# Performance work log

Measured on AMD Instinct MI355X. Metric: run time of the kernel, lower is better.

## Reference

```python
import jax, jax.numpy as jnp
import numpy as np

B = 128
IN = 256
NLVL = 6
KLVL = 3
CH = 4
C = 4 * CH * CH          # 64 channels per node
OU = 8                   # out_filter_siz_u
OV = 8                   # out_filter_siz_v
NK = 2 ** KLVL           # 8 leaf nodes per axis
W_SCALE = 1.0 / 16.0     # ~1/sqrt(2*2*C) so 7 stacked relu-convs stay numerically sane


def setup_inputs() -> dict:
    key = jax.random.key(0)
    ks = jax.random.split(key, 2 * NLVL + 4)
    fx = IN // 2 ** NLVL  # 4: input patch filter size
    inp = {}
    inp["in_data"] = jax.random.normal(ks[0], (B, IN, IN, 1), jnp.float32)
    inp["in_filter"] = jax.random.normal(ks[1], (fx, fx, 1, C), jnp.float32) * W_SCALE
    inp["in_bias"] = jnp.zeros((C,), jnp.float32)
    i = 2
    for lvl in range(1, NLVL + 1):
        n = 2 ** min(lvl, KLVL)  # node grid: grows to 2^klvl then stays
        inp[f"f{lvl}"] = jax.random.normal(ks[i], (n, n, 2, 2, C, C), jnp.float32) * W_SCALE
        inp[f"b{lvl}"] = jnp.zeros((n, n, C), jnp.float32)
        i += 1
    inp["Wd"] = jax.random.normal(ks[i], (NK, NK, 2, C, OU * OV), jnp.float32) * W_SCALE
    return inp


def _node_conv(x, w, b):
    # x: [Nu,Nv,B,H,W,C]; w: [Nu,Nv,2,2,C,C]; 2x2 stride-2 VALID conv per node
    Nu, Nv, Bn, H, W, Cc = x.shape
    xr = x.reshape(Nu, Nv, Bn, H // 2, 2, W // 2, 2, Cc)
    y = jnp.einsum('uvbhxwyc,uvxyco->uvbhwo', xr, w)
    return jax.nn.relu(y + b[:, :, None, None, None, :])


def _forward(in_data, in_filter, in_bias, fs, bs, Wd):
    Bn = in_data.shape[0]
    fx, fy = in_filter.shape[0], in_filter.shape[1]
    # input interp conv: stride == kernel -> non-overlapping patch GEMM
    xr = in_data[..., 0].reshape(Bn, in_data.shape[1] // fx, fx, in_data.shape[2] // fy, fy)
    x = jax.nn.relu(jnp.einsum('bxpyq,pqc->bxyc', xr, in_filter[:, :, 0, :]) + in_bias)
    x = x[None, None]  # [1,1,B,2^nlvl,2^nlvl,C] node grid
    for lvl in range(1, NLVL + 1):
        if lvl <= KLVL:
            # children (itu,itv) read parent (itu//2, itv//2)
            x = jnp.repeat(jnp.repeat(x, 2, axis=0), 2, axis=1)
        x = _node_conv(x, fs[lvl - 1], bs[lvl - 1])
    feats = x[:, :, :, 0, 0, :]  # [NK,NK,B,C]; spatial is 1x1 at level nlvl
    out = jnp.einsum('uvbc,uvrck->uvbrk', feats, Wd)  # r in {real, imag}
    out = out.reshape(NK, NK, Bn, 2, OU, OV)
    out = jnp.transpose(out, (2, 0, 4, 1, 5, 3))  # [B,itu,ou,itv,ov,2]
    return out.reshape(Bn, NK * OU, NK * OV, 2)


def reference(in_data, in_filter, in_bias, f1, b1, f2, b2, f3, b3, f4, b4, f5, b5, f6, b6, Wd):
    fs = (f1, f2, f3, f4, f5, f6)
    bs = (b1, b2, b3, b4, b5, b6)
    return _forward(in_data, in_filter, in_bias, fs, bs, Wd)
```

## Files before the change

### kernel.cpp

```cpp
#include <hip/hip_runtime.h>
#include <hip/hip_bf16.h>
#include <cstdint>
#include <cstddef>


typedef __attribute__((ext_vector_type(8))) short short8;
typedef __attribute__((ext_vector_type(4))) float f32x4;
typedef unsigned short ushort_t;

static __device__ __forceinline__ float b2f(const __hip_bfloat16 x) {
    return __bfloat162float(x);
}
static __device__ __forceinline__ ushort_t f2bf(float x) {
    __hip_bfloat16 h = __float2bfloat16(x);
    ushort_t u;
    __builtin_memcpy(&u, &h, 2);
    return u;
}
static __device__ __forceinline__ void gl_lds16(const void* g, void* l) {
    __builtin_amdgcn_global_load_lds(
        (const __attribute__((address_space(1))) void*)g,
        (__attribute__((address_space(3))) void*)l, 16, 0, 0);
}
#define WAIT_LGKM0() __builtin_amdgcn_s_waitcnt(0xC07F)
#define WAIT_VM0()   __builtin_amdgcn_s_waitcnt(0x0F70)

#define PREP_BLOCKS 2533

static __device__ __forceinline__ void prep_work(
    int gid, int isbf,
    const void* f1, const void* f2, const void* f3,
    const void* f4, const void* f5, const void* f6, const void* wdsrc,
    const void* b1, const void* b2, const void* b3,
    const void* b4, const void* b5, const void* b6,
    ushort_t* __restrict__ wbuf, ushort_t* __restrict__ wdbuf,
    float* __restrict__ bbuf)
{
    if (gid >= 648448) return;
    if (gid >= 630784) {
        const int bg = gid - 630784;
        const void* src; int base;
        if      (bg <   256) { src = b1; base = 0;     }
        else if (bg <  1280) { src = b2; base = 256;   }
        else if (bg <  5376) { src = b3; base = 1280;  }
        else if (bg <  9472) { src = b4; base = 5376;  }
        else if (bg < 13568) { src = b5; base = 9472;  }
        else                 { src = b6; base = 13568; }
        const int local = bg - base;
        bbuf[bg] = isbf ? b2f(((const __hip_bfloat16*)src)[local])
                        : ((const float*)src)[local];
        return;
    }
    if (gid >= 565248) {
        const int local = gid - 565248;
        const int lane = local & 63;
        const int slot = (local >> 6) & 15;
        const int site = local >> 10;
        const int ks2 = slot >> 3, nh = slot & 7, q = lane >> 4;
        const int n = nh * 16 + (lane & 15);
        const int r = n >> 6, kk = n & 63;
        const int cbase = ks2 * 32 + q * 8;
        ushort_t pk[8];
        if (isbf) {
            const ushort_t* s = (const ushort_t*)wdsrc;
            #pragma unroll
            for (int j = 0; j < 8; j++)
                pk[j] = s[(((size_t)(site * 2 + r) * 64 + cbase + j) * 64) + kk];
        } else {
            const float* s = (const float*)wdsrc;
            #pragma unroll
            for (int j = 0; j < 8; j++)
                pk[j] = f2bf(s[(((size_t)(site * 2 + r) * 64 + cbase + j) * 64) + kk]);
        }
        *(uint4*)&wdbuf[(size_t)local * 8] = *(uint4*)pk;
        return;
    }
    const void* fsrc; int base;
    if      (gid <   8192) { fsrc = f1; base = 0;      }
    else if (gid <  40960) { fsrc = f2; base = 8192;   }
    else if (gid < 172032) { fsrc = f3; base = 40960;  }
    else if (gid < 303104) { fsrc = f4; base = 172032; }
    else if (gid < 434176) { fsrc = f5; base = 303104; }
    else                   { fsrc = f6; base = 434176; }
    const int local = gid - base;
    const int lane = local & 63;
    const int slot = (local >> 6) & 7;
    const int sitetap = local >> 9;
    const int ks = slot >> 2, nh = slot & 3, q = lane >> 4;
    const int n = (lane & 15) + nh * 16;
    const int kbase = ks * 32 + q * 8;
    ushort_t pk[8];
    if (isbf) {
        const ushort_t* s = (const ushort_t*)fsrc + (size_t)sitetap * 4096;
        #pragma unroll
        for (int j = 0; j < 8; j++) pk[j] = s[(kbase + j) * 64 + n];
    } else {
        const float* s = (const float*)fsrc + (size_t)sitetap * 4096;
        #pragma unroll
        for (int j = 0; j < 8; j++) pk[j] = f2bf(s[(kbase + j) * 64 + n]);
    }
    *(uint4*)&wbuf[(size_t)gid * 8] = *(uint4*)pk;
}

static __device__ __forceinline__ void stage0_body(
    int blk, int isbf,
    const void* __restrict__ in_data, const void* __restrict__ filt,
    const void* __restrict__ bias, __hip_bfloat16* __restrict__ x0,
    int b_off, int Bc)
{
    const int X  = blk & 63;
    const int bl = blk >> 6;
    const int bg = bl + b_off;

    __shared__ float sIn[4][256];
    __shared__ float sF[16][64];
    __shared__ float sB[64];

    const int t = threadIdx.x;
    const size_t srow = ((size_t)bg * 256 + (size_t)X * 4) * 256;

    if (isbf) {
        const __hip_bfloat16* src = (const __hip_bfloat16*)in_data + srow;
        #pragma unroll
        for (int i = 0; i < 4; i++) {
            int flat = i * 256 + t;
            int p = flat >> 8, col = flat & 255;
            sIn[p][col] = b2f(src[(size_t)p * 256 + col]);
        }
        const __hip_bfloat16* fsrc = (const __hip_bfloat16*)filt;
        #pragma unroll
        for (int i = 0; i < 4; i++) {
            int flat = i * 256 + t;
            sF[flat >> 6][flat & 63] = b2f(fsrc[flat]);
        }
        if (t < 64) sB[t] = b2f(((const __hip_bfloat16*)bias)[t]);
    } else {
        const float* src = (const float*)in_data + srow;
        const int p = t >> 6, c4 = (t & 63) * 4;
        *(float4*)&sIn[p][c4] = *(const float4*)(src + (size_t)p * 256 + c4);
        const float* fsrc = (const float*)filt;
        #pragma unroll
        for (int i = 0; i < 4; i++) {
            int flat = i * 256 + t;
            sF[flat >> 6][flat & 63] = fsrc[flat];
        }
        if (t < 64) sB[t] = ((const float*)bias)[t];
    }
    __syncthreads();

    const int ty = t >> 4;
    const int tc = t & 15;

    float acc[4][4];
    {
        const float4 bv = *(const float4*)&sB[tc * 4];
        #pragma unroll
        for (int yi = 0; yi < 4; yi++) {
            acc[yi][0] = bv.x; acc[yi][1] = bv.y;
            acc[yi][2] = bv.z; acc[yi][3] = bv.w;
        }
    }

    #pragma unroll
    for (int p = 0; p < 4; p++) {
        float4 rin[4], rf[4];
        #pragma unroll
        for (int yi = 0; yi < 4; yi++)
            rin[yi] = *(const float4*)&sIn[p][ty * 16 + yi * 4];
        #pragma unroll
        for (int q = 0; q < 4; q++)
            rf[q] = *(const float4*)&sF[p * 4 + q][tc * 4];
        #pragma unroll
        for (int yi = 0; yi < 4; yi++) {
            #pragma unroll
            for (int q = 0; q < 4; q++) {
                const float a = ((const float*)&rin[yi])[q];
                acc[yi][0] = fmaf(a, rf[q].x, acc[yi][0]);
                acc[yi][1] = fmaf(a, rf[q].y, acc[yi][1]);
                acc[yi][2] = fmaf(a, rf[q].z, acc[yi][2]);
                acc[yi][3] = fmaf(a, rf[q].w, acc[yi][3]);
            }
        }
    }

    ushort_t* dst = (ushort_t*)x0;
    #pragma unroll
    for (int yi = 0; yi < 4; yi++) {
        uint2 pk;
        pk.x = (uint32_t)f2bf(fmaxf(acc[yi][0], 0.f))
             | ((uint32_t)f2bf(fmaxf(acc[yi][1], 0.f)) << 16);
        pk.y = (uint32_t)f2bf(fmaxf(acc[yi][2], 0.f))
             | ((uint32_t)f2bf(fmaxf(acc[yi][3], 0.f)) << 16);
        const int wpos = ty * 4 + yi;
        *(uint2*)(dst + ((size_t)(X * 64 + wpos) * Bc + bl) * 64 + tc * 4) = pk;
    }
}

__global__ __launch_bounds__(256) void k_prep0(
    const void* __restrict__ in_data,
    const void* f1, const void* f2, const void* f3,
    const void* f4, const void* f5, const void* f6, const void* wdsrc,
    const void* b1, const void* b2, const void* b3,
    const void* b4, const void* b5, const void* b6,
    ushort_t* __restrict__ wbuf, ushort_t* __restrict__ wdbuf,
    float* __restrict__ bbuf, int* __restrict__ flag,
    const void* __restrict__ filt, const void* __restrict__ bias0,
    __hip_bfloat16* __restrict__ x0, int Bc)
{
    __shared__ int sflag;
    const int t = threadIdx.x;
    if (t < 64) {
        const float v = __uint_as_float(((const uint32_t*)in_data)[t]);
        const bool plaus = (v == 0.0f) || (fabsf(v) > 1e-8f && fabsf(v) < 1e4f);
        const unsigned long long m = __ballot(plaus);
        if (t == 0) sflag = (__popcll(m) >= 48) ? 0 : 1;
    }
    __syncthreads();
    const int isbf = sflag;

    if (blockIdx.x < PREP_BLOCKS) {
        if (blockIdx.x == 0 && t == 0) *flag = isbf;
        prep_work(blockIdx.x * 256 + t, isbf,
                  f1, f2, f3, f4, f5, f6, wdsrc,
                  b1, b2, b3, b4, b5, b6, wbuf, wdbuf, bbuf);
    } else {
        stage0_body(blockIdx.x - PREP_BLOCKS, isbf, in_data, filt, bias0, x0, 0, Bc);
    }
}

__global__ __launch_bounds__(256) void k_stage0(
    const void* __restrict__ in_data, const void* __restrict__ filt,
    const void* __restrict__ bias, __hip_bfloat16* __restrict__ x0,
    const int* __restrict__ flag, int b_off, int Bc)
{
    stage0_body(blockIdx.x, *flag, in_data, filt, bias, x0, b_off, Bc);
}

__global__ __launch_bounds__(256, 2) void k_level4(
    const __hip_bfloat16* __restrict__ xin,
    const ushort_t* __restrict__ wbuf,
    const float* __restrict__ bbuf,
    __hip_bfloat16* __restrict__ xout,
    int Nv_out, int HW, int Bc, int mtiles)
{
    __shared__ ushort_t smem[17408];

    int idx = blockIdx.x;
    const int mt = idx % mtiles; idx /= mtiles;
    const int w  = idx % HW; idx /= HW;
    const int h  = idx % HW; idx /= HW;
    const int Nv_in = Nv_out >> 1;
    const int vp = idx % Nv_in;
    const int up = idx / Nv_in;

    const int t = threadIdx.x;
    const int wave = t >> 6, lane = t & 63;
    const int lm = lane & 15, lq = lane >> 4;

    const int so = (2 * up + (wave >> 1)) * Nv_out + (2 * vp + (wave & 1));
    const int H_in = HW * 2;
    const size_t pstride = (size_t)Bc * 64;
    const size_t siteb = (size_t)(up * Nv_in + vp) * H_in * H_in * pstride;
    const ushort_t* wsite = wbuf + (size_t)so * 4 * 4096 + lane * 8;

    {
        const int hi = 2 * h + (wave >> 1), wi = 2 * w + (wave & 1);
        const size_t tapoff = siteb + ((size_t)hi * H_in + wi) * pstride;
        #pragma unroll
        for (int j = 0; j < 8; j++) {
            const int ks = j >> 2, mh = j & 3;
            int b = mt * 64 + mh * 16 + lm;
            if (b >= Bc) b = Bc - 1;
            gl_lds16(xin + tapoff + (size_t)b * 64 + ks * 32 + lq * 8,
                     &smem[(wave * 8 + j) * 512]);
        }
    }

    short8 breg[32];
    #pragma unroll
    for (int s = 0; s < 32; s++)
        breg[s] = *(const short8*)(wsite + s * 512);

    float bv[4];
    #pragma unroll
    for (int fn = 0; fn < 4; fn++) bv[fn] = bbuf[so * 64 + fn * 16 + lm];

    __syncthreads();

    const f32x4 zero = {0.f, 0.f, 0.f, 0.f};
    f32x4 acc[4][4];
    #pragma unroll
    for (int i = 0; i < 4; i++)
        #pragma unroll
        for (int j = 0; j < 4; j++) acc[i][j] = zero;

    #pragma unroll
    for (int tap = 0; tap < 4; tap++) {
        #pragma unroll
        for (int ks = 0; ks < 2; ks++) {
            #pragma unroll
            for (int fm = 0; fm < 4; fm++) {
                short8 a = *(const short8*)&smem[(tap * 8 + ks * 4 + fm) * 512 + lane * 8];
                #pragma unroll
                for (int fn = 0; fn < 4; fn++)
                    acc[fm][fn] = __builtin_amdgcn_mfma_f32_16x16x32_bf16(
                        a, breg[tap * 8 + ks * 4 + fn], acc[fm][fn], 0, 0, 0);
            }
        }
    }
    __syncthreads();

    ushort_t* so_buf = smem + wave * 4352;
    #pragma unroll
    for (int fm = 0; fm < 4; fm++) {
        #pragma unroll
        for (int fn = 0; fn < 4; fn++) {
            #pragma unroll
            for (int r = 0; r < 4; r++) {
                const int row = fm * 16 + lq * 4 + r;
                so_buf[row * 68 + fn * 16 + lm] =
                    f2bf(fmaxf(acc[fm][fn][r] + bv[fn], 0.f));
            }
        }
    }
    __syncthreads();

    const size_t obase = ((size_t)so * HW * HW + (size_t)h * HW + w) * pstride;
    #pragma unroll
    for (int i = 0; i < 8; i++) {
        const int task = i * 64 + lane;
        const int oct = task & 7, row = task >> 3;
        const int b = mt * 64 + row;
        if (b < Bc) {
            *(uint4*)(xout + obase + (size_t)b * 64 + oct * 8) =
                *(const uint4*)&so_buf[row * 68 + oct * 8];
        }
    }
}

__global__ __launch_bounds__(256) void k_f456(
    const __hip_bfloat16* __restrict__ xin,
    const ushort_t* __restrict__ w4, const ushort_t* __restrict__ w5,
    const ushort_t* __restrict__ w6, const ushort_t* __restrict__ wd,
    const float* __restrict__ b4, const float* __restrict__ b5,
    const float* __restrict__ b6,
    void* __restrict__ out, const int* __restrict__ flag,
    int Bc, int b_off, int mtiles)
{
    const int isbf = *flag;
    const int bx = blockIdx.x;
    const int mt = bx % mtiles;
    const int site = bx / mtiles;
    const int u = site >> 3, v = site & 7;

    __shared__ ushort_t smem[37376];

    const int t = threadIdx.x;
    const int wv = t >> 6, lane = t & 63;
    const int lm = lane & 15, lq = lane >> 4;

    const ushort_t* w6s = w6 + (size_t)site * 16384 + lane * 8;
    const ushort_t* wds = wd + (size_t)site * 8192  + lane * 8;

    float bv4[4], bv5[4];
    #pragma unroll
    for (int fn = 0; fn < 4; fn++) {
        bv4[fn] = b4[site * 64 + fn * 16 + lm];
        bv5[fn] = b5[site * 64 + fn * 16 + lm];
    }
    const float bv6 = b6[site * 64 + wv * 16 + lm];

    {
        const ushort_t* w4s = w4 + (size_t)site * 16384;
        #pragma unroll
        for (int s2 = 0; s2 < 8; s2++) {
            const int s = wv * 8 + s2;
            gl_lds16(w4s + s * 512 + lane * 8, &smem[s * 512]);
        }
    }
    __syncthreads();

    const f32x4 zero = {0.f, 0.f, 0.f, 0.f};
    const int h5 = wv >> 1, w5p = wv & 1;
    ushort_t* mid1w = smem + 16384 + wv * 4224;
    ushort_t* Aw = smem + 33280 + wv * 1024;
    const size_t pstride = (size_t)Bc * 64;

    int brow = mt * 16 + lm;
    if (brow >= Bc) brow = Bc - 1;
    const __hip_bfloat16* xbase =
        xin + (size_t)site * 64 * pstride + (size_t)brow * 64 + lq * 8;

    for (int i = 0; i < 4; i++) {
        const int h4 = 2 * h5 + (i >> 1), w4p = 2 * w5p + (i & 1);
        f32x4 acc[4];
        #pragma unroll
        for (int b_ = 0; b_ < 4; b_++) acc[b_] = zero;

        for (int tap = 0; tap < 4; tap++) {
            const int h3 = 2 * h4 + (tap >> 1), w3 = 2 * w4p + (tap & 1);
            const size_t poff = (size_t)(h3 * 8 + w3) * pstride;
            WAIT_LGKM0();
            #pragma unroll
            for (int ks = 0; ks < 2; ks++) {
                gl_lds16(xbase + poff + ks * 32, &Aw[ks * 512]);
            }
            WAIT_VM0();
            __builtin_amdgcn_sched_barrier(0);
            #pragma unroll
            for (int ks = 0; ks < 2; ks++) {
                short8 a = *(const short8*)&Aw[ks * 512 + lane * 8];
                #pragma unroll
                for (int fn = 0; fn < 4; fn++) {
                    short8 bfr = *(const short8*)&smem[(tap * 8 + ks * 4 + fn) * 512 + lane * 8];
                    acc[fn] = __builtin_amdgcn_mfma_f32_16x16x32_bf16(a, bfr, acc[fn], 0, 0, 0);
                }
            }
        }
        #pragma unroll
        for (int fn = 0; fn < 4; fn++) {
            #pragma unroll
            for (int r = 0; r < 4; r++) {
                const int m = lq * 4 + r;
                const int ch = fn * 16 + lm;
                mid1w[m * 264 + i * 64 + ch] =
                    f2bf(fmaxf(acc[fn][r] + bv4[fn], 0.f));
            }
        }
    }
    __syncthreads();

    {
        const ushort_t* w5s = w5 + (size_t)site * 16384;
        #pragma unroll
        for (int s2 = 0; s2 < 8; s2++) {
            const int s = wv * 8 + s2;
            gl_lds16(w5s + s * 512 + lane * 8, &smem[s * 512]);
        }
    }
    __syncthreads();

    short8 b3r[8];
    short8 wdr[4];
    {
        f32x4 acc2[4];
        #pragma unroll
        for (int b_ = 0; b_ < 4; b_++) acc2[b_] = zero;

        #pragma unroll
        for (int i = 0; i < 4; i++) {
            #pragma unroll
            for (int ks = 0; ks < 2; ks++) {
                short8 a0 = *(const short8*)&mid1w[lm * 264 + i * 64 + ks * 32 + lq * 8];
                #pragma unroll
                for (int fn = 0; fn < 4; fn++) {
                    short8 bfr = *(const short8*)&smem[(i * 8 + ks * 4 + fn) * 512 + lane * 8];
                    acc2[fn] = __builtin_amdgcn_mfma_f32_16x16x32_bf16(a0, bfr, acc2[fn], 0, 0, 0);
                }
            }
        }

        #pragma unroll
        for (int tap = 0; tap < 4; tap++)
            #pragma unroll
            for (int ks = 0; ks < 2; ks++)
                b3r[tap * 2 + ks] = *(const short8*)(w6s + (tap * 8 + ks * 4 + wv) * 512);
        #pragma unroll
        for (int ks = 0; ks < 2; ks++)
            #pragma unroll
            for (int n2 = 0; n2 < 2; n2++)
                wdr[ks * 2 + n2] = *(const short8*)(wds + (ks * 8 + 2 * wv + n2) * 512);

        #pragma unroll
        for (int fn = 0; fn < 4; fn++) {
            #pragma unroll
            for (int r = 0; r < 4; r++) {
                const int m = lq * 4 + r;
                const int ch = fn * 16 + lm;
                mid1w[m * 72 + ch] =
                    f2bf(fmaxf(acc2[fn][r] + bv5[fn], 0.f));
            }
        }
    }
    __syncthreads();

    {
        f32x4 acc3 = zero;
        #pragma unroll
        for (int tap = 0; tap < 4; tap++) {
            const ushort_t* sl = smem + 16384 + tap * 4224;
            #pragma unroll
            for (int ks = 0; ks < 2; ks++) {
                short8 a0 = *(const short8*)&sl[lm * 72 + ks * 32 + lq * 8];
                acc3 = __builtin_amdgcn_mfma_f32_16x16x32_bf16(a0, b3r[tap * 2 + ks], acc3, 0, 0, 0);
            }
        }
        ushort_t* mid3 = smem + 33280;
        #pragma unroll
        for (int r = 0; r < 4; r++) {
            const int m = lq * 4 + r;
            const int ch = wv * 16 + lm;
            mid3[m * 72 + ch] = f2bf(fmaxf(acc3[r] + bv6, 0.f));
        }
    }
    __syncthreads();

    {
        const ushort_t* mid3 = smem + 33280;
        f32x4 acc4[2];
        acc4[0] = zero; acc4[1] = zero;
        #pragma unroll
        for (int ks = 0; ks < 2; ks++) {
            short8 a0 = *(const short8*)&mid3[lm * 72 + ks * 32 + lq * 8];
            #pragma unroll
            for (int n2 = 0; n2 < 2; n2++) {
                acc4[n2] = __builtin_amdgcn_mfma_f32_16x16x32_bf16(a0, wdr[ks * 2 + n2], acc4[n2], 0, 0, 0);
            }
        }
        #pragma unroll
        for (int n2 = 0; n2 < 2; n2++) {
            const int n = (2 * wv + n2) * 16 + lm;
            const int rr = n >> 6, ou = (n >> 3) & 7, ov = n & 7;
            const size_t obase =
                (((size_t)(u * 8 + ou)) * 64 + (v * 8 + ov)) * 2 + rr;
            #pragma unroll
            for (int reg = 0; reg < 4; reg++) {
                const int brw = mt * 16 + lq * 4 + reg;
                if (brw < Bc) {
                    const size_t oidx = obase + (size_t)(b_off + brw) * 8192;
                    if (isbf) ((__hip_bfloat16*)out)[oidx] =
                        __float2bfloat16(acc4[n2][reg]);
                    else ((float*)out)[oidx] = acc4[n2][reg];
                }
            }
        }
    }
}

extern "C" void kernel_launch(void* const* d_in, const int* in_sizes, int n_in,
                              void* d_out, int out_size, void* d_ws, size_t ws_size,
                              hipStream_t stream)
{
    (void)in_sizes; (void)n_in; (void)out_size;

    const void* in_data = d_in[0];
    const void* filt    = d_in[1];
    const void* bias0   = d_in[2];
    const void* fl[7];
    const void* bl[7];
    for (int l = 1; l <= 6; l++) {
        fl[l] = d_in[1 + 2 * l];
        bl[l] = d_in[2 + 2 * l];
    }
    const void* Wd = d_in[15];

    const int Bfull = 128;
    const size_t perB = (size_t)64 * 64 * 64;

    const size_t wbufBytes  = 565248ull * 16;
    const size_t wdbufBytes = 65536ull * 16;
    const size_t bbufBytes  = 17664ull * 4;
    const size_t headBytes  = 256 + wbufBytes + wdbufBytes + bbufBytes;

    const size_t avail = ws_size > headBytes ? ws_size - headBytes : 0;
    int Bc = 0;
    for (int c = 128; c >= 1; c >>= 1) {
        if ((size_t)2 * c * perB * sizeof(__hip_bfloat16) <= avail) { Bc = c; break; }
    }
    if (Bc == 0) return;

    int* flag = (int*)d_ws;
    ushort_t* wbuf  = (ushort_t*)((char*)d_ws + 256);
    ushort_t* wdbuf = (ushort_t*)((char*)d_ws + 256 + wbufBytes);
    float* bbuf = (float*)((char*)d_ws + 256 + wbufBytes + wdbufBytes);
    __hip_bfloat16* bufA = (__hip_bfloat16*)((char*)d_ws + headBytes);
    __hip_bfloat16* bufB = bufA + (size_t)Bc * perB;

    static const size_t w_off[7] = {0, 0, 65536, 327680, 1376256, 2424832, 3473408};
    static const int    b_off_tab[7] = {0, 0, 256, 1280, 5376, 9472, 13568};

    const int mt4 = (Bc + 63) / 64;
    const int mt16 = (Bc + 15) / 16;

    for (int b_off = 0; b_off < Bfull; b_off += Bc) {
        if (b_off == 0) {
            k_prep0<<<dim3(PREP_BLOCKS + Bc * 64), 256, 0, stream>>>(
                in_data,
                fl[1], fl[2], fl[3], fl[4], fl[5], fl[6], Wd,
                bl[1], bl[2], bl[3], bl[4], bl[5], bl[6],
                wbuf, wdbuf, bbuf, flag,
                filt, bias0, bufA, Bc);
        } else {
            k_stage0<<<dim3(Bc * 64), 256, 0, stream>>>(in_data, filt, bias0, bufA, flag, b_off, Bc);
        }

        __hip_bfloat16* cur = bufA;
        __hip_bfloat16* nxt = bufB;
        for (int lvl = 1; lvl <= 3; lvl++) {
            const int Nu = 1 << lvl;
            const int H  = 64 >> lvl;
            const int Nv_in = Nu >> 1;
            dim3 grid(Nv_in * Nv_in * H * H * mt4);
            k_level4<<<grid, 256, 0, stream>>>(cur, wbuf + w_off[lvl],
                bbuf + b_off_tab[lvl], nxt, Nu, H, Bc, mt4);
            __hip_bfloat16* tmp = cur; cur = nxt; nxt = tmp;
        }

        k_f456<<<dim3(64 * mt16), 256, 0, stream>>>(cur,
            wbuf + w_off[4], wbuf + w_off[5], wbuf + w_off[6], wdbuf,
            bbuf + b_off_tab[4], bbuf + b_off_tab[5], bbuf + b_off_tab[6],
            d_out, flag, Bc, b_off, mt16);
    }
}
```

Baseline: 249.2 us.

## Fuse tree levels 1 and 2 into one kernel via LDS intermediate

Adds a k_fused12 kernel that computes level-1 and level-2 node convolutions in one pass. Each block loads a 4x4 spatial patch of stage-0 output, keeps the level-1 results in LDS, and then computes the 16 level-2 sites directly. This removes one kernel launch and the global write and re-read of the level-1 activations. In exchange the block uses more LDS, holds 32 weight fragments in registers per wave, and uses smaller 16-row batch tiles, which could lower occupancy.

```diff
diff --git a/kernel.cpp b/kernel.cpp
--- a/kernel.cpp
+++ b/kernel.cpp
@@ -236,6 +236,143 @@
     stage0_body(blockIdx.x, *flag, in_data, filt, bias, x0, b_off, Bc);
 }
 
+__global__ __launch_bounds__(256, 2) void k_fused12(
+    const __hip_bfloat16* __restrict__ xin,
+    const ushort_t* __restrict__ w1,
+    const ushort_t* __restrict__ w2,
+    const float* __restrict__ b1, const float* __restrict__ b2,
+    __hip_bfloat16* __restrict__ xout,
+    int Bc, int mtiles)
+{
+    __shared__ __align__(16) ushort_t smem[34816];
+
+    int idx = blockIdx.x;
+    const int mt = idx % mtiles; idx /= mtiles;
+    const int w2p = idx & 15;
+    const int h2p = idx >> 4;
+
+    const int t = threadIdx.x;
+    const int wave = t >> 6, lane = t & 63;
+    const int lm = lane & 15, lq = lane >> 4;
+
+    const size_t pstride = (size_t)Bc * 64;
+
+    {
+        int brow = mt * 16 + lm;
+        if (brow >= Bc) brow = Bc - 1;
+        #pragma unroll
+        for (int k = 0; k < 4; k++) {
+            const int p = wave * 4 + k;
+            const int i = p >> 2, j = p & 3;
+            const size_t poff =
+                ((size_t)(4 * h2p + i) * 64 + (4 * w2p + j)) * pstride;
+            #pragma unroll
+            for (int ks = 0; ks < 2; ks++) {
+                gl_lds16(xin + poff + (size_t)brow * 64 + ks * 32 + lq * 8,
+                         &smem[(p * 2 + ks) * 512]);
+            }
+        }
+    }
+
+    const ushort_t* w1site = w1 + (size_t)wave * 16384 + lane * 8;
+    short8 breg[32];
+    #pragma unroll
+    for (int s = 0; s < 32; s++) breg[s] = *(const short8*)(w1site + s * 512);
+
+    float bv1[4];
+    #pragma unroll
+    for (int fn = 0; fn < 4; fn++) bv1[fn] = b1[wave * 64 + fn * 16 + lm];
+
+    __syncthreads();
+
+    const f32x4 zero = {0.f, 0.f, 0.f, 0.f};
+    ushort_t* l1b = smem + 16384;
+
+    #pragma unroll
+    for (int ab = 0; ab < 4; ab++) {
+        const int a = ab >> 1, b = ab & 1;
+        f32x4 acc[4];
+        #pragma unroll
+        for (int fn = 0; fn < 4; fn++) acc[fn] = zero;
+
+        #pragma unroll
+        for (int cd = 0; cd < 4; cd++) {
+            const int p = (2 * a + (cd >> 1)) * 4 + (2 * b + (cd & 1));
+            #pragma unroll
+            for (int ks = 0; ks < 2; ks++) {
+                short8 afr = *(const short8*)&smem[(p * 2 + ks) * 512 + lane * 8];
+                #pragma unroll
+                for (int fn = 0; fn < 4; fn++)
+                    acc[fn] = __builtin_amdgcn_mfma_f32_16x16x32_bf16(
+                        afr, breg[cd * 8 + ks * 4 + fn], acc[fn], 0, 0, 0);
+            }
+        }
+        ushort_t* dst = l1b + (wave * 4 + ab) * 1152;
+        #pragma unroll
+        for (int fn = 0; fn < 4; fn++) {
+            #pragma unroll
+            for (int r = 0; r < 4; r++) {
+                const int m = lq * 4 + r;
+                dst[m * 72 + fn * 16 + lm] =
+                    f2bf(fmaxf(acc[fn][r] + bv1[fn], 0.f));
+            }
+        }
+    }
+    __syncthreads();
+
+    ushort_t* so_buf = smem + wave * 2176;
+    for (int k = 0; k < 4; k++) {
+        const int s2 = wave * 4 + k;
+        const int u2 = s2 >> 2, v2 = s2 & 3;
+        const int s1p = (u2 >> 1) * 2 + (v2 >> 1);
+        const ushort_t* w2site = w2 + (size_t)s2 * 16384 + lane * 8;
+
+        f32x4 acc[4];
+        #pragma unroll
+        for (int fn = 0; fn < 4; fn++) acc[fn] = zero;
+
+        #pragma unroll
+        for (int ab = 0; ab < 4; ab++) {
+            const ushort_t* sl = l1b + (s1p * 4 + ab) * 1152;
+            #pragma unroll
+            for (int ks = 0; ks < 2; ks++) {
+                short8 afr = *(const short8*)&sl[lm * 72 + ks * 32 + lq * 8];
+                #pragma unroll
+                for (int fn = 0; fn < 4; fn++) {
+                    short8 bfr = *(const short8*)(w2site + (ab * 8 + ks * 4 + fn) * 512);
+                    acc[fn] = __builtin_amdgcn_mfma_f32_16x16x32_bf16(
+                        afr, bfr, acc[fn], 0, 0, 0);
+                }
+            }
+        }
+
+        float bv2[4];
+        #pragma unroll
+        for (int fn = 0; fn < 4; fn++) bv2[fn] = b2[s2 * 64 + fn * 16 + lm];
+
+        #pragma unroll
+        for (int fn = 0; fn < 4; fn++) {
+            #pragma unroll
+            for (int r = 0; r < 4; r++) {
+                const int m = lq * 4 + r;
+                so_buf[m * 68 + fn * 16 + lm] =
+                    f2bf(fmaxf(acc[fn][r] + bv2[fn], 0.f));
+            }
+        }
+        const size_t obase = ((size_t)s2 * 256 + h2p * 16 + w2p) * pstride;
+        #pragma unroll
+        for (int i2 = 0; i2 < 2; i2++) {
+            const int task = i2 * 64 + lane;
+            const int oct = task & 7, row = task >> 3;
+            const int brw = mt * 16 + row;
+            if (brw < Bc) {
+                *(uint4*)(xout + obase + (size_t)brw * 64 + oct * 8) =
+                    *(const uint4*)&so_buf[row * 68 + oct * 8];
+            }
+        }
+    }
+}
+
 __global__ __launch_bounds__(256, 2) void k_level4(
     const __hip_bfloat16* __restrict__ xin,
     const ushort_t* __restrict__ wbuf,
@@ -243,7 +380,7 @@
     __hip_bfloat16* __restrict__ xout,
     int Nv_out, int HW, int Bc, int mtiles)
 {
-    __shared__ ushort_t smem[17408];
+    __shared__ __align__(16) ushort_t smem[17408];
 
     int idx = blockIdx.x;
     const int mt = idx % mtiles; idx /= mtiles;
@@ -353,7 +490,7 @@
     const int site = bx / mtiles;
     const int u = site >> 3, v = site & 7;
 
-    __shared__ ushort_t smem[37376];
+    __shared__ __align__(16) ushort_t smem[37376];
 
     const int t = threadIdx.x;
     const int wv = t >> 6, lane = t & 63;
@@ -576,10 +713,7 @@
     __hip_bfloat16* bufA = (__hip_bfloat16*)((char*)d_ws + headBytes);
     __hip_bfloat16* bufB = bufA + (size_t)Bc * perB;
 
-    static const size_t w_off[7] = {0, 0, 65536, 327680, 1376256, 2424832, 3473408};
-    static const int    b_off_tab[7] = {0, 0, 256, 1280, 5376, 9472, 13568};
-
-    const int mt4 = (Bc + 63) / 64;
+    const int mt4  = (Bc + 63) / 64;
     const int mt16 = (Bc + 15) / 16;
 
     for (int b_off = 0; b_off < Bfull; b_off += Bc) {
@@ -594,21 +728,18 @@
             k_stage0<<<dim3(Bc * 64), 256, 0, stream>>>(in_data, filt, bias0, bufA, flag, b_off, Bc);
         }
 
-        __hip_bfloat16* cur = bufA;
-        __hip_bfloat16* nxt = bufB;
-        for (int lvl = 1; lvl <= 3; lvl++) {
-            const int Nu = 1 << lvl;
-            const int H  = 64 >> lvl;
-            const int Nv_in = Nu >> 1;
-            dim3 grid(Nv_in * Nv_in * H * H * mt4);
-            k_level4<<<grid, 256, 0, stream>>>(cur, wbuf + w_off[lvl],
-                bbuf + b_off_tab[lvl], nxt, Nu, H, Bc, mt4);
-            __hip_bfloat16* tmp = cur; cur = nxt; nxt = tmp;
-        }
-
-        k_f456<<<dim3(64 * mt16), 256, 0, stream>>>(cur,
-            wbuf + w_off[4], wbuf + w_off[5], wbuf + w_off[6], wdbuf,
-            bbuf + b_off_tab[4], bbuf + b_off_tab[5], bbuf + b_off_tab[6],
+        k_fused12<<<dim3(256 * mt16), 256, 0, stream>>>(
+            bufA, wbuf, wbuf + 65536, bbuf, bbuf + 256, bufB, Bc, mt16);
+
+        {
+            dim3 grid(4 * 4 * 8 * 8 * mt4);
+            k_level4<<<grid, 256, 0, stream>>>(bufB, wbuf + 327680,
+                bbuf + 1280, bufA, 8, 8, Bc, mt4);
+        }
+
+        k_f456<<<dim3(64 * mt16), 256, 0, stream>>>(bufA,
+            wbuf + 1376256, wbuf + 2424832, wbuf + 3473408, wdbuf,
+            bbuf + 5376, bbuf + 9472, bbuf + 13568,
             d_out, flag, Bc, b_off, mt16);
     }
 }
```

New measurement: 248.8 us. Within noise of the previous version (-0.1%).
